# Kernel tuning notes

Hardware: AMD Instinct MI355X
Metric: run time of the kernel (lower is better)

The kernel has to match this reference:

```python
import jax, jax.numpy as jnp
import numpy as np

B, F, T, K = 16, 256, 2048, 20
TEMP = 0.5
EPS = 1e-8  # torch cosine_similarity eps


def setup_inputs() -> dict:
    key = jax.random.key(0)
    k1, k2, k3 = jax.random.split(key, 3)
    z = jax.random.normal(k1, (B, F, T), dtype=jnp.float32)
    c = jax.random.normal(k2, (B, F, T + 1), dtype=jnp.float32)
    # torch: torch.randint(0, full_len - 1, size=(B, T * K))  -> values in [0, T-2]
    negative_inds = jax.random.randint(k3, (B, T * K), 0, T - 1, dtype=jnp.int64)
    return {"z": z, "c": c, "negative_inds": negative_inds}


def reference(z, c, negative_inds):
    # ---- _generate_negatives ----
    # z: [B, F, T] -> flat rows [B*T, F]
    z_flat = jnp.transpose(z, (0, 2, 1)).reshape(-1, F)
    # per-batch offset i*T (torch adds it in-place for i in 1..B-1)
    inds = negative_inds + (jnp.arange(B, dtype=negative_inds.dtype) * T)[:, None]
    negatives = z_flat[inds.reshape(-1)].reshape(B, T, K, F)

    # ---- _calculate_similarity ----
    c_t = jnp.transpose(c[..., 1:], (0, 2, 1))[:, :, None, :]  # [B, T, 1, F] (drop start token)
    z_t = jnp.transpose(z, (0, 2, 1))[:, :, None, :]           # [B, T, 1, F]
    neg_is_pos = jnp.all(c_t == negatives, axis=-1)            # [B, T, K]
    targets = jnp.concatenate([c_t, negatives], axis=-2)       # [B, T, K+1, F]

    num = jnp.sum(z_t * targets, axis=-1)                      # [B, T, K+1]
    denom = jnp.maximum(
        jnp.linalg.norm(z_t, axis=-1) * jnp.linalg.norm(targets, axis=-1), EPS
    )
    logits = (num / denom) / TEMP                              # [B, T, K+1]

    # mask negatives that exactly equal the positive (wav2vec2-style)
    pad = jnp.zeros_like(neg_is_pos[..., :1])
    full_mask = jnp.concatenate([pad, neg_is_pos], axis=-1)    # [B, T, K+1]
    logits = jnp.where(full_mask, -jnp.inf, logits)

    return logits.reshape(-1, K + 1)                           # [B*T, K+1]
```

## Files before the change

kernel.cpp:

```cpp
#include <hip/hip_runtime.h>
#include <hip/hip_fp16.h>
#include <math.h>

#define B_ 16
#define F_ 256
#define T_ 2048
#define K_ 20
#define OUTK 21
#define NPAIR 10

typedef _Float16 half2v __attribute__((ext_vector_type(2)));
typedef float v2f __attribute__((ext_vector_type(2)));

#if __has_builtin(__builtin_amdgcn_cvt_pk_f32_fp8) && __has_builtin(__builtin_amdgcn_cvt_pk_fp8_f32)
#define HW_FP8 1
#else
#define HW_FP8 0
#endif

#if !HW_FP8
__device__ __forceinline__ float dec_fp8(unsigned v) {
    unsigned s = (v >> 7) & 1, e = (v >> 3) & 15, m = v & 7;
    float r = e ? __uint_as_float(((e + 120u) << 23) | (m << 20))
                : (float)m * 0.001953125f;
    return s ? -r : r;
}
__device__ __forceinline__ unsigned enc_fp8(float x) {
    unsigned bits = __float_as_uint(x);
    unsigned s = bits >> 31;
    unsigned a = bits & 0x7fffffffu;
    float ax = __uint_as_float(a);
    unsigned r;
    if (ax < 0.015625f) {
        r = (unsigned)(int)(ax * 512.f + 0.5f);
    } else {
        int e = (int)(a >> 23) - 127;
        unsigned m = a & 0x7fffffu;
        unsigned keep = m >> 20, rest = m & 0xFFFFFu;
        keep += (rest > 0x80000u) || (rest == 0x80000u && (keep & 1));
        if (keep == 8) { keep = 0; ++e; }
        r = ((unsigned)(e + 7) << 3) | keep;
    }
    return (s << 7) | r;
}
#endif

__device__ __forceinline__ unsigned pack_fp8x4(float a0, float a1, float a2, float a3) {
#if HW_FP8
    int u = 0;
    u = __builtin_amdgcn_cvt_pk_fp8_f32(a0, a1, u, false);
    u = __builtin_amdgcn_cvt_pk_fp8_f32(a2, a3, u, true);
    return (unsigned)u;
#else
    return enc_fp8(a0) | (enc_fp8(a1) << 8) | (enc_fp8(a2) << 16) | (enc_fp8(a3) << 24);
#endif
}
template <bool HI>
__device__ __forceinline__ v2f unpk_fp8(unsigned u) {
#if HW_FP8
    return __builtin_amdgcn_cvt_pk_f32_fp8((int)u, HI);
#else
    v2f r; unsigned x = HI ? (u >> 16) : u;
    r[0] = dec_fp8(x & 0xFF); r[1] = dec_fp8((x >> 8) & 0xFF);
    return r;
#endif
}

__global__ __launch_bounds__(256) void prep_kernel(
    const float* __restrict__ z, const float* __restrict__ c,
    ushort* __restrict__ zth, unsigned char* __restrict__ zf8,
    unsigned char* __restrict__ cf8, float* __restrict__ out)
{
    __shared__ float tz[256][33];
    __shared__ float tc[256][33];
    __shared__ float scz[32], scc[32];
    int b  = blockIdx.y;
    int t0 = blockIdx.x * 32;
    const float* zb = z + (size_t)b * F_ * T_;
    const float* cb = c + (size_t)b * F_ * (T_ + 1);
    int tl = threadIdx.x & 31;
    int fl = threadIdx.x >> 5;
#pragma unroll
    for (int i = 0; i < 32; ++i) {
        int f = i * 8 + fl;
        tz[f][tl] = zb[(size_t)f * T_ + t0 + tl];
    }
#pragma unroll
    for (int i = 0; i < 32; ++i) {
        int f = i * 8 + fl;
        tc[f][tl] = cb[(size_t)f * (T_ + 1) + t0 + tl + 1];
    }
    __syncthreads();
    if (threadIdx.x < 32) {
        float zn = 0.f, cn = 0.f, zc = 0.f;
#pragma unroll 8
        for (int f = 0; f < 256; ++f) {
            float a = tz[f][threadIdx.x], d = tc[f][threadIdx.x];
            zn = fmaf(a, a, zn); cn = fmaf(d, d, cn); zc = fmaf(a, d, zc);
        }
        float nz_ = sqrtf(zn), nc_ = sqrtf(cn);
        scz[threadIdx.x] = (nz_ > 0.f) ? (1.0f / nz_) : 0.f;
        scc[threadIdx.x] = (nc_ > 0.f) ? (1.0f / nc_) : 0.f;
        int bt = (b << 11) + t0 + threadIdx.x;
        out[(size_t)bt * OUTK] = (zc / fmaxf(nz_ * nc_, 1e-8f)) * 2.0f;
    }
    __syncthreads();
    {
        int l = threadIdx.x & 127, rhi = threadIdx.x >> 7;
#pragma unroll
        for (int j2 = 0; j2 < 16; ++j2) {
            int row = j2 * 2 + rhi;
            float s = scz[row];
            float a  = tz[2 * l][row] * s;
            float bb = tz[2 * l + 1][row] * s;
            unsigned u = ((unsigned)__half_as_ushort(__float2half(bb)) << 16)
                       |  (unsigned)__half_as_ushort(__float2half(a));
            ((unsigned*)(zth + ((size_t)b * T_ + t0 + row) * F_))[l] = u;
        }
    }
    {
        int j = threadIdx.x & 63, r4 = threadIdx.x >> 6;
#pragma unroll
        for (int it = 0; it < 8; ++it) {
            int row = it * 4 + r4;
            float sz_ = scz[row], sc_ = scc[row];
            unsigned uz = pack_fp8x4(tz[4 * j][row] * sz_, tz[4 * j + 1][row] * sz_,
                                     tz[4 * j + 2][row] * sz_, tz[4 * j + 3][row] * sz_);
            unsigned uc = pack_fp8x4(tc[4 * j][row] * sc_, tc[4 * j + 1][row] * sc_,
                                     tc[4 * j + 2][row] * sc_, tc[4 * j + 3][row] * sc_);
            ((unsigned*)(zf8 + ((size_t)b * T_ + t0 + row) * F_))[j] = uz;
            ((unsigned*)(cf8 + ((size_t)b * T_ + t0 + row) * F_))[j] = uc;
        }
    }
}

__device__ __forceinline__ float dpp_half_sum(float x) {
    x += __int_as_float(__builtin_amdgcn_mov_dpp(__float_as_int(x), 0x111, 0xF, 0xF, true));
    x += __int_as_float(__builtin_amdgcn_mov_dpp(__float_as_int(x), 0x112, 0xF, 0xF, true));
    x += __int_as_float(__builtin_amdgcn_mov_dpp(__float_as_int(x), 0x114, 0xF, 0xF, true));
    x += __int_as_float(__builtin_amdgcn_mov_dpp(__float_as_int(x), 0x118, 0xF, 0xF, true));
    x += __int_as_float(__builtin_amdgcn_mov_dpp(__float_as_int(x), 0x142, 0xF, 0xF, true));
    return x;
}

__global__ __launch_bounds__(256, 8) void sim_kernel(
    const ushort* __restrict__ zth, const unsigned char* __restrict__ zf8,
    const unsigned char* __restrict__ cf8, const int* __restrict__ inds,
    float* __restrict__ out)
{
    __shared__ float sd[128];
    int i = blockIdx.x;
    int b = (i & 7) | ((i >= 4096) ? 8 : 0);
    int wid = threadIdx.x >> 6;
    int t = (((i >> 3) & 511) << 2) + wid;
    int lane = threadIdx.x & 63;
    int hl = lane & 31;
    int hi = lane >> 5;
    int bt = __builtin_amdgcn_readfirstlane((b << 11) + t);

    const int* myinds = inds + bt * K_;
    int idxv = myinds[(lane < K_) ? lane : 0];

    uint4 zv  = ((const uint4*)(zth + (size_t)bt * F_))[hl];
    uint2 cv8 = ((const uint2*)(cf8 + (size_t)bt * F_))[hl];

    const char* tbl8 = (const char*)zf8;
    unsigned zbase8  = (unsigned)(b << 11) * 256u;
    unsigned laneoff = (unsigned)hl * 8u;

    uint2 tv[NPAIR];
#pragma unroll
    for (int p = 0; p < NPAIR; ++p) {
        unsigned ilo = (unsigned)__builtin_amdgcn_readlane(idxv, 2 * p);
        unsigned ihi = (unsigned)__builtin_amdgcn_readlane(idxv, 2 * p + 1);
        unsigned off = zbase8 + (hi ? ihi : ilo) * 256u + laneoff;
        tv[p] = *(const uint2*)(tbl8 + off);
    }

    __builtin_amdgcn_sched_barrier(0);

    float zf[8];
    {
        unsigned uu[4] = {zv.x, zv.y, zv.z, zv.w};
#pragma unroll
        for (int q = 0; q < 4; ++q) {
            half2v h = __builtin_bit_cast(half2v, uu[q]);
            zf[2 * q] = (float)h[0]; zf[2 * q + 1] = (float)h[1];
        }
    }

    float dz[NPAIR];
#pragma unroll
    for (int p = 0; p < NPAIR; ++p) {
        v2f t01 = unpk_fp8<false>(tv[p].x);
        v2f t23 = unpk_fp8<true >(tv[p].x);
        v2f t45 = unpk_fp8<false>(tv[p].y);
        v2f t67 = unpk_fp8<true >(tv[p].y);
        float d = zf[0] * t01[0];
        d = fmaf(zf[1], t01[1], d);
        d = fmaf(zf[2], t23[0], d);
        d = fmaf(zf[3], t23[1], d);
        d = fmaf(zf[4], t45[0], d);
        d = fmaf(zf[5], t45[1], d);
        d = fmaf(zf[6], t67[0], d);
        d = fmaf(zf[7], t67[1], d);
        dz[p] = d;
    }

    unsigned mb = 0;
#pragma unroll
    for (int p = 0; p < NPAIR; ++p) {
        unsigned long long ball = __ballot(tv[p].x == cv8.x);
        unsigned blo = (unsigned)ball, bhi = (unsigned)(ball >> 32);
        if (blo == 0xFFFFFFFFu || bhi == 0xFFFFFFFFu) {
            bool full = (tv[p].x == cv8.x) && (tv[p].y == cv8.y);
            unsigned long long b2 = __ballot(full);
            if ((unsigned)b2 == 0xFFFFFFFFu)          mb |= 1u << (1 + 2 * p);
            if ((unsigned)(b2 >> 32) == 0xFFFFFFFFu)  mb |= 1u << (2 + 2 * p);
        }
    }

#pragma unroll
    for (int p = 0; p < NPAIR; ++p) dz[p] = dpp_half_sum(dz[p]);

    if (hl == 31) {
#pragma unroll
        for (int p = 0; p < NPAIR; ++p) sd[wid * 32 + 1 + 2 * p + hi] = dz[p];
    }

    if (lane >= 1 && lane < OUTK) {
        float v = sd[wid * 32 + lane] * 2.0f;
        if ((mb >> lane) & 1u) v = -INFINITY;
        out[(size_t)bt * OUTK + lane] = v;
    }
}

extern "C" void kernel_launch(void* const* d_in, const int* in_sizes, int n_in,
                              void* d_out, int out_size, void* d_ws, size_t ws_size,
                              hipStream_t stream)
{
    const float* z    = (const float*)d_in[0];
    const float* c    = (const float*)d_in[1];
    const int*   inds = (const int*)d_in[2];
    float* out = (float*)d_out;

    char* ws = (char*)d_ws;
    size_t f16_bytes = (size_t)B_ * T_ * F_ * sizeof(ushort);
    size_t f8_bytes  = (size_t)B_ * T_ * F_;
    ushort* zth = (ushort*)ws;
    unsigned char* zf8 = (unsigned char*)(ws + f16_bytes);
    unsigned char* cf8 = (unsigned char*)(ws + f16_bytes + f8_bytes);

    dim3 tb(256), tg(T_ / 32, B_);
    prep_kernel<<<tg, tb, 0, stream>>>(z, c, zth, zf8, cf8, out);
    sim_kernel<<<dim3(B_ * T_ / 4), dim3(256), 0, stream>>>(zth, zf8, cf8, inds, out);
}
```

Before: 52.24 us.

## Split prep kernel into separate z and c blocks; compute positive logit in sim kernel

The prep kernel now launches twice as many blocks, each transposing and normalizing only z or only c, which halves shared memory per block so more blocks can reside per CU. Because z and c no longer share a block, the positive cosine logit is no longer computed in prep. The sim kernel computes it from the fp16 z row and the fp8 c row with an extra dot product and reduction. This lowers the precision of the positive logit, since c is now quantized to fp8 before the product.

```diff
diff --git a/kernel.cpp b/kernel.cpp
--- a/kernel.cpp
+++ b/kernel.cpp
@@ -45,14 +45,11 @@
 }
 #endif
 
-__device__ __forceinline__ unsigned pack_fp8x4(float a0, float a1, float a2, float a3) {
+__device__ __forceinline__ unsigned pack_fp8x2(float a0, float a1) {
 #if HW_FP8
-    int u = 0;
-    u = __builtin_amdgcn_cvt_pk_fp8_f32(a0, a1, u, false);
-    u = __builtin_amdgcn_cvt_pk_fp8_f32(a2, a3, u, true);
-    return (unsigned)u;
+    return (unsigned)__builtin_amdgcn_cvt_pk_fp8_f32(a0, a1, 0, false) & 0xFFFFu;
 #else
-    return enc_fp8(a0) | (enc_fp8(a1) << 8) | (enc_fp8(a2) << 16) | (enc_fp8(a3) << 24);
+    return enc_fp8(a0) | (enc_fp8(a1) << 8);
 #endif
 }
 template <bool HI>
@@ -69,67 +66,58 @@
 __global__ __launch_bounds__(256) void prep_kernel(
     const float* __restrict__ z, const float* __restrict__ c,
     ushort* __restrict__ zth, unsigned char* __restrict__ zf8,
-    unsigned char* __restrict__ cf8, float* __restrict__ out)
+    unsigned char* __restrict__ cf8)
 {
-    __shared__ float tz[256][33];
-    __shared__ float tc[256][33];
-    __shared__ float scz[32], scc[32];
+    __shared__ float tile[256][33];
+    __shared__ float sc[32];
+    int which = blockIdx.z;
+    const float* src = which ? c : z;
+    int Lsrc = which ? (T_ + 1) : T_;
+    int co   = which;
+
     int b  = blockIdx.y;
     int t0 = blockIdx.x * 32;
-    const float* zb = z + (size_t)b * F_ * T_;
-    const float* cb = c + (size_t)b * F_ * (T_ + 1);
+    const float* srcb = src + (size_t)b * F_ * Lsrc;
     int tl = threadIdx.x & 31;
     int fl = threadIdx.x >> 5;
 #pragma unroll
     for (int i = 0; i < 32; ++i) {
         int f = i * 8 + fl;
-        tz[f][tl] = zb[(size_t)f * T_ + t0 + tl];
-    }
-#pragma unroll
-    for (int i = 0; i < 32; ++i) {
-        int f = i * 8 + fl;
-        tc[f][tl] = cb[(size_t)f * (T_ + 1) + t0 + tl + 1];
+        tile[f][tl] = srcb[(size_t)f * Lsrc + (t0 + tl + co)];
     }
     __syncthreads();
     if (threadIdx.x < 32) {
-        float zn = 0.f, cn = 0.f, zc = 0.f;
+        float s = 0.f;
 #pragma unroll 8
-        for (int f = 0; f < 256; ++f) {
-            float a = tz[f][threadIdx.x], d = tc[f][threadIdx.x];
-            zn = fmaf(a, a, zn); cn = fmaf(d, d, cn); zc = fmaf(a, d, zc);
-        }
-        float nz_ = sqrtf(zn), nc_ = sqrtf(cn);
-        scz[threadIdx.x] = (nz_ > 0.f) ? (1.0f / nz_) : 0.f;
-        scc[threadIdx.x] = (nc_ > 0.f) ? (1.0f / nc_) : 0.f;
-        int bt = (b << 11) + t0 + threadIdx.x;
-        out[(size_t)bt * OUTK] = (zc / fmaxf(nz_ * nc_, 1e-8f)) * 2.0f;
+        for (int f = 0; f < 256; ++f) { float v = tile[f][threadIdx.x]; s += v * v; }
+        float n = sqrtf(s);
+        sc[threadIdx.x] = (n > 0.f) ? (1.0f / n) : 0.f;
     }
     __syncthreads();
-    {
-        int l = threadIdx.x & 127, rhi = threadIdx.x >> 7;
+    int l   = threadIdx.x & 127;
+    int rhi = threadIdx.x >> 7;
+    if (which == 0) {
 #pragma unroll
         for (int j2 = 0; j2 < 16; ++j2) {
             int row = j2 * 2 + rhi;
-            float s = scz[row];
-            float a  = tz[2 * l][row] * s;
-            float bb = tz[2 * l + 1][row] * s;
+            float s  = sc[row];
+            float a  = tile[2 * l][row] * s;
+            float bb = tile[2 * l + 1][row] * s;
             unsigned u = ((unsigned)__half_as_ushort(__float2half(bb)) << 16)
                        |  (unsigned)__half_as_ushort(__float2half(a));
             ((unsigned*)(zth + ((size_t)b * T_ + t0 + row) * F_))[l] = u;
-        }
-    }
-    {
-        int j = threadIdx.x & 63, r4 = threadIdx.x >> 6;
-#pragma unroll
-        for (int it = 0; it < 8; ++it) {
-            int row = it * 4 + r4;
-            float sz_ = scz[row], sc_ = scc[row];
-            unsigned uz = pack_fp8x4(tz[4 * j][row] * sz_, tz[4 * j + 1][row] * sz_,
-                                     tz[4 * j + 2][row] * sz_, tz[4 * j + 3][row] * sz_);
-            unsigned uc = pack_fp8x4(tc[4 * j][row] * sc_, tc[4 * j + 1][row] * sc_,
-                                     tc[4 * j + 2][row] * sc_, tc[4 * j + 3][row] * sc_);
-            ((unsigned*)(zf8 + ((size_t)b * T_ + t0 + row) * F_))[j] = uz;
-            ((unsigned*)(cf8 + ((size_t)b * T_ + t0 + row) * F_))[j] = uc;
+            ((ushort*)(zf8 + ((size_t)b * T_ + t0 + row) * F_))[l] =
+                (ushort)pack_fp8x2(a, bb);
+        }
+    } else {
+#pragma unroll
+        for (int j2 = 0; j2 < 16; ++j2) {
+            int row = j2 * 2 + rhi;
+            float s  = sc[row];
+            float a  = tile[2 * l][row] * s;
+            float bb = tile[2 * l + 1][row] * s;
+            ((ushort*)(cf8 + ((size_t)b * T_ + t0 + row) * F_))[l] =
+                (ushort)pack_fp8x2(a, bb);
         }
     }
 }
@@ -189,6 +177,23 @@
         }
     }
 
+    float dc;
+    {
+        v2f c01 = unpk_fp8<false>(cv8.x);
+        v2f c23 = unpk_fp8<true >(cv8.x);
+        v2f c45 = unpk_fp8<false>(cv8.y);
+        v2f c67 = unpk_fp8<true >(cv8.y);
+        float d = zf[0] * c01[0];
+        d = fmaf(zf[1], c01[1], d);
+        d = fmaf(zf[2], c23[0], d);
+        d = fmaf(zf[3], c23[1], d);
+        d = fmaf(zf[4], c45[0], d);
+        d = fmaf(zf[5], c45[1], d);
+        d = fmaf(zf[6], c67[0], d);
+        d = fmaf(zf[7], c67[1], d);
+        dc = d;
+    }
+
     float dz[NPAIR];
 #pragma unroll
     for (int p = 0; p < NPAIR; ++p) {
@@ -220,15 +225,17 @@
         }
     }
 
+    dc = dpp_half_sum(dc);
 #pragma unroll
     for (int p = 0; p < NPAIR; ++p) dz[p] = dpp_half_sum(dz[p]);
 
     if (hl == 31) {
+        if (hi == 0) sd[wid * 32] = dc;
 #pragma unroll
         for (int p = 0; p < NPAIR; ++p) sd[wid * 32 + 1 + 2 * p + hi] = dz[p];
     }
 
-    if (lane >= 1 && lane < OUTK) {
+    if (lane < OUTK) {
         float v = sd[wid * 32 + lane] * 2.0f;
         if ((mb >> lane) & 1u) v = -INFINITY;
         out[(size_t)bt * OUTK + lane] = v;
@@ -251,7 +258,7 @@
     unsigned char* zf8 = (unsigned char*)(ws + f16_bytes);
     unsigned char* cf8 = (unsigned char*)(ws + f16_bytes + f8_bytes);
 
-    dim3 tb(256), tg(T_ / 32, B_);
-    prep_kernel<<<tg, tb, 0, stream>>>(z, c, zth, zf8, cf8, out);
+    dim3 tb(256), tg(T_ / 32, B_, 2);
+    prep_kernel<<<tg, tb, 0, stream>>>(z, c, zth, zf8, cf8);
     sim_kernel<<<dim3(B_ * T_ / 4), dim3(256), 0, stream>>>(zth, zf8, cf8, inds, out);
 }
```

Measured after the change: 46.76 us. -10.5%, faster.
